# Optimization experiments

Measured on AMD Instinct MI355X. Metric: run time of the kernel, lower is better.

Reference implementation:

```python
import jax, jax.numpy as jnp
import numpy as np

B, L, QD, H, D = 2, 2048, 1024, 16, 64  # batch, seq, q_dim, heads, head_dim
INNER = H * D


def rms_norm(x, scale):
    # matches torch RMSNorm: mean over last dim in fp32, eps=1e-6, learned scale
    rrms = jax.lax.rsqrt(jnp.mean(x.astype(jnp.float32) ** 2, axis=-1, keepdims=True) + 1e-6)
    return (x * rrms).astype(x.dtype) * scale


def apply_rope(xq, xk, pe):
    # pe: [1,1,L,D//2,2,2] rotation-matrix pairs (FLUX-style)
    def rot(x):
        xs = x.reshape(*x.shape[:-1], D // 2, 1, 2)  # B H L D/2 1 2
        out = pe[..., 0] * xs[..., 0] + pe[..., 1] * xs[..., 1]  # B H L D/2 2
        return out.reshape(x.shape).astype(x.dtype)
    return rot(xq), rot(xk)


def setup_inputs() -> dict:
    key = jax.random.key(0)
    ks = jax.random.split(key, 6)
    s = 0.02
    return {
        "x": jax.random.normal(ks[0], (B, L, QD), jnp.float32),
        "pe": jax.random.normal(ks[1], (1, 1, L, D // 2, 2, 2), jnp.float32),
        "Wq": jax.random.normal(ks[2], (INNER, QD), jnp.float32) * s,
        "Wkv": jax.random.normal(ks[3], (2 * INNER, QD), jnp.float32) * s,
        "Wproj": jax.random.normal(ks[4], (QD, INNER), jnp.float32) * s,
        "bproj": jnp.zeros((QD,), jnp.float32),
        "q_scale": jnp.ones((D,), jnp.float32),
        "k_scale": jnp.ones((D,), jnp.float32),
    }


def reference(x, pe, Wq, Wkv, Wproj, bproj, q_scale, k_scale):
    # q/kv projections (self-attention: context = x)
    q = jnp.einsum('blc,ec->ble', x, Wq).reshape(B, L, H, D).transpose(0, 2, 1, 3)  # B H L D
    kv = jnp.einsum('blc,ec->ble', x, Wkv).reshape(B, L, 2, H, D)  # layout (K H D)
    k = kv[:, :, 0].transpose(0, 2, 1, 3)  # B H L D
    v = kv[:, :, 1].transpose(0, 2, 1, 3)  # B H L D
    # per-head QK RMSNorm
    q = rms_norm(q, q_scale)
    k = rms_norm(k, k_scale)
    # RoPE then scaled dot-product attention
    q, k = apply_rope(q, k, pe)
    scores = jnp.einsum('bhqd,bhkd->bhqk', q, k) / np.float32(np.sqrt(D))
    attn = jax.nn.softmax(scores, axis=-1)
    o = jnp.einsum('bhqk,bhkd->bhqd', attn, v)
    o = o.transpose(0, 2, 1, 3).reshape(B, L, INNER)  # B L (H D)
    return o @ Wproj.T + bproj
```

## Files before the change

### kernel.cpp

```cpp
#include <hip/hip_runtime.h>
#include <hip/hip_bf16.h>
#include <stdint.h>

#define BB 2
#define LL 2048
#define QDIM 1024
#define NH 16
#define HD 64

using bf16x8 = __attribute__((ext_vector_type(8))) __bf16;
using f32x4  = __attribute__((ext_vector_type(4))) float;
using u16x8  = __attribute__((ext_vector_type(8))) unsigned short;
using u32x2  = __attribute__((ext_vector_type(2))) uint32_t;

__device__ __forceinline__ unsigned short f2bf(float f) {
  uint32_t u = __builtin_bit_cast(uint32_t, f);
  u = (u + 0x7fffu + ((u >> 16) & 1u)) >> 16;
  return (unsigned short)u;
}
__device__ __forceinline__ float bf2f(unsigned short h) {
  uint32_t u = ((uint32_t)h) << 16;
  return __builtin_bit_cast(float, u);
}

__device__ __forceinline__ void gload_lds16(const void* g, void* l) {
  __builtin_amdgcn_global_load_lds((__attribute__((address_space(1))) void*)g,
                                   (__attribute__((address_space(3))) void*)l,
                                   16, 0, 0);
}

__global__ __launch_bounds__(256) void k_cast_bf16(const float* __restrict__ in,
                                                   unsigned short* __restrict__ out, int n) {
  int i = (blockIdx.x * 256 + threadIdx.x) * 8;
  if (i >= n) return;
  float4 a = *reinterpret_cast<const float4*>(in + i);
  float4 b = *reinterpret_cast<const float4*>(in + i + 4);
  u16x8 o;
  o[0] = f2bf(a.x); o[1] = f2bf(a.y); o[2] = f2bf(a.z); o[3] = f2bf(a.w);
  o[4] = f2bf(b.x); o[5] = f2bf(b.y); o[6] = f2bf(b.z); o[7] = f2bf(b.w);
  *reinterpret_cast<u16x8*>(out + i) = o;
}

template <int MODE>
__global__ __launch_bounds__(256) void k_gemm_bt(const unsigned short* __restrict__ A,
                                                 const unsigned short* __restrict__ Bw,
                                                 unsigned short* __restrict__ Cb,
                                                 float* __restrict__ Cf,
                                                 unsigned short* __restrict__ vT,
                                                 const float* __restrict__ bias,
                                                 int K, int ldc) {
  __shared__ unsigned short As[128 * 32];
  __shared__ unsigned short Bs[128 * 32];
  const int t = threadIdx.x;
  const int lane = t & 63, w = t >> 6;
  const int wm = w >> 1, wn = w & 1;
  const int g = lane >> 4, r16 = lane & 15;
  const size_t am0 = (size_t)blockIdx.x * 128;
  const size_t bn0 = (size_t)blockIdx.y * 128;

  f32x4 acc[4][4] = {};

  const int o0 = t * 16;
  const int row0 = o0 >> 6, cb0 = o0 & 63;
  const int o1 = 4096 + t * 16;
  const int row1 = o1 >> 6, cb1 = o1 & 63;

  for (int kb = 0; kb < K; kb += 32) {
    __syncthreads();
    gload_lds16(A  + (am0 + row0) * K + kb + (cb0 >> 1), (char*)As + o0);
    gload_lds16(A  + (am0 + row1) * K + kb + (cb1 >> 1), (char*)As + o1);
    gload_lds16(Bw + (bn0 + row0) * K + kb + (cb0 >> 1), (char*)Bs + o0);
    gload_lds16(Bw + (bn0 + row1) * K + kb + (cb1 >> 1), (char*)Bs + o1);
    __syncthreads();

    bf16x8 af[4], bfr[4];
#pragma unroll
    for (int i = 0; i < 4; ++i)
      af[i] = *reinterpret_cast<const bf16x8*>((const char*)As + (wm * 64 + i * 16 + r16) * 64 + g * 16);
#pragma unroll
    for (int j = 0; j < 4; ++j)
      bfr[j] = *reinterpret_cast<const bf16x8*>((const char*)Bs + (wn * 64 + j * 16 + r16) * 64 + g * 16);
#pragma unroll
    for (int i = 0; i < 4; ++i)
#pragma unroll
      for (int j = 0; j < 4; ++j)
        acc[i][j] = __builtin_amdgcn_mfma_f32_16x16x32_bf16(af[i], bfr[j], acc[i][j], 0, 0, 0);
  }

#pragma unroll
  for (int i = 0; i < 4; ++i)
#pragma unroll
    for (int j = 0; j < 4; ++j) {
      size_t row = am0 + wm * 64 + i * 16 + g * 4;
      int col = (int)bn0 + wn * 64 + j * 16 + r16;
      if (MODE == 2) {
#pragma unroll
        for (int r = 0; r < 4; ++r) Cf[(row + r) * ldc + col] = acc[i][j][r] + bias[col];
      } else if (MODE == 0) {
#pragma unroll
        for (int r = 0; r < 4; ++r) Cb[(row + r) * ldc + col] = f2bf(acc[i][j][r]);
      } else {
        if (col < 1024) {
#pragma unroll
          for (int r = 0; r < 4; ++r) Cb[(row + r) * 2048 + 1024 + col] = f2bf(acc[i][j][r]);
        } else {
          int e = col - 1024, h = e >> 6, d = e & 63;
          int b = (int)(row >> 11), l2 = (int)(row & 2047);
          ushort4 pk;
          pk.x = f2bf(acc[i][j][0]); pk.y = f2bf(acc[i][j][1]);
          pk.z = f2bf(acc[i][j][2]); pk.w = f2bf(acc[i][j][3]);
          *reinterpret_cast<ushort4*>(vT + ((size_t)(b * 16 + h) * 64 + d) * 2048 + l2) = pk;
        }
      }
    }
}

__global__ __launch_bounds__(256) void k_norm_rope(unsigned short* __restrict__ qkbuf,
                                                   const float* __restrict__ pe,
                                                   const float* __restrict__ qs,
                                                   const float* __restrict__ ks) {
  const int row = blockIdx.x;
  const int l = row & (LL - 1);
  const int t = threadIdx.x, w = t >> 6, lane = t & 63;
  const int hgrp = lane >> 5, dp = lane & 31;
  const size_t base = (size_t)row * 2048;
  const float4 pev = *reinterpret_cast<const float4*>(pe + ((size_t)l * 32 + dp) * 4);
  const float2 qsv = *reinterpret_cast<const float2*>(qs + dp * 2);
  const float2 ksv = *reinterpret_cast<const float2*>(ks + dp * 2);

#pragma unroll
  for (int pass = 0; pass < 4; ++pass) {
    const int isK = pass >> 1;
    const int h = w * 4 + (pass & 1) * 2 + hgrp;
    unsigned short* p = qkbuf + base + isK * 1024 + h * 64 + dp * 2;
    uint32_t v = *reinterpret_cast<uint32_t*>(p);
    float xe = bf2f((unsigned short)(v & 0xffff)), xo = bf2f((unsigned short)(v >> 16));
    float s = xe * xe + xo * xo;
#pragma unroll
    for (int mk = 1; mk < 32; mk <<= 1) s += __shfl_xor(s, mk);
    float rr = rsqrtf(s * (1.0f / 64.0f) + 1e-6f);
    float sx = isK ? ksv.x : qsv.x, sy = isK ? ksv.y : qsv.y;
    float ne = xe * rr * sx, no = xo * rr * sy;
    float oe = pev.x * ne + pev.y * no;
    float oo = pev.z * ne + pev.w * no;
    *reinterpret_cast<uint32_t*>(p) = (uint32_t)f2bf(oe) | ((uint32_t)f2bf(oo) << 16);
  }
}

__global__ __launch_bounds__(256, 4) void k_flash(const unsigned short* __restrict__ qkbuf,
                                                  const unsigned short* __restrict__ vT,
                                                  unsigned short* __restrict__ ob) {
  __shared__ unsigned short Plds[4][16][64];
  __shared__ unsigned short Ktile[2][64 * 64];
  __shared__ unsigned short Vtile[2][64 * 64];
  const int t = threadIdx.x, w = t >> 6, lane = t & 63;
  const int g = lane >> 4, r16 = lane & 15;
  const int id = blockIdx.x;
  const int bh = (id & 7) + (((id >> 3) & 3) << 3);
  const int lt = id >> 5;
  const int b = bh >> 4, h = bh & 15;
  const int l0 = lt * 64 + w * 16;
  const size_t qkb = (size_t)b * LL * 2048;
  const unsigned short* Qp = qkbuf + qkb + (size_t)(l0 + r16) * 2048 + h * 64;
  const unsigned short* Kbase = qkbuf + qkb + 1024 + h * 64;
  const unsigned short* Vbase = vT + (size_t)bh * 64 * 2048;

  const bf16x8 qf0 = *reinterpret_cast<const bf16x8*>(Qp + g * 8);
  const bf16x8 qf1 = *reinterpret_cast<const bf16x8*>(Qp + 32 + g * 8);

  f32x4 oacc[4] = {};
  float m = -1e30f, lsum = 0.f;

  char* Pw = (char*)&Plds[w][0][0];
  const int pswz = (r16 & 7) << 4;
  const int prow = r16 * 128;
  const int wr0 = prow + ((0 * 32 + g * 8) ^ pswz);
  const int wr1 = prow + ((1 * 32 + g * 8) ^ pswz);
  const int wr2 = prow + ((2 * 32 + g * 8) ^ pswz);
  const int wr3 = prow + ((3 * 32 + g * 8) ^ pswz);
  const int rd0 = prow + ((g * 16) ^ pswz);
  const int rd1 = prow + ((64 + g * 16) ^ pswz);

  const int so0 = t * 16, sr0 = so0 >> 7, sl0 = (so0 & 127) ^ ((sr0 & 7) << 4);
  const int so1 = 4096 + t * 16, sr1 = so1 >> 7, sl1 = (so1 & 127) ^ ((sr1 & 7) << 4);

  gload_lds16(Kbase + (size_t)sr0 * 2048 + (sl0 >> 1), (char*)&Ktile[0][0] + so0);
  gload_lds16(Kbase + (size_t)sr1 * 2048 + (sl1 >> 1), (char*)&Ktile[0][0] + so1);
  gload_lds16(Vbase + (size_t)sr0 * 2048 + (sl0 >> 1), (char*)&Vtile[0][0] + so0);
  gload_lds16(Vbase + (size_t)sr1 * 2048 + (sl1 >> 1), (char*)&Vtile[0][0] + so1);
  __syncthreads();

  const int kswz = (r16 & 7) << 4;

  for (int kt = 0; kt < LL; kt += 64) {
    const int cur = (kt >> 6) & 1;
    if (kt + 64 < LL) {
      const int nxt = cur ^ 1;
      gload_lds16(Kbase + (size_t)(kt + 64 + sr0) * 2048 + (sl0 >> 1), (char*)&Ktile[nxt][0] + so0);
      gload_lds16(Kbase + (size_t)(kt + 64 + sr1) * 2048 + (sl1 >> 1), (char*)&Ktile[nxt][0] + so1);
      gload_lds16(Vbase + (size_t)sr0 * 2048 + kt + 64 + (sl0 >> 1), (char*)&Vtile[nxt][0] + so0);
      gload_lds16(Vbase + (size_t)sr1 * 2048 + kt + 64 + (sl1 >> 1), (char*)&Vtile[nxt][0] + so1);
    }
    const char* Kt = (const char*)&Ktile[cur][0];
    const char* Vt = (const char*)&Vtile[cur][0];

    f32x4 s[4];
#pragma unroll
    for (int kb = 0; kb < 4; ++kb) {
      const char* kp = Kt + (kb * 16 + r16) * 128;
      bf16x8 ka0 = *reinterpret_cast<const bf16x8*>(kp + ((g * 16) ^ kswz));
      bf16x8 ka1 = *reinterpret_cast<const bf16x8*>(kp + ((64 + g * 16) ^ kswz));
      f32x4 z = {};
      z = __builtin_amdgcn_mfma_f32_16x16x32_bf16(ka0, qf0, z, 0, 0, 0);
      z = __builtin_amdgcn_mfma_f32_16x16x32_bf16(ka1, qf1, z, 0, 0, 0);
      s[kb] = z;
    }
    float p[16];
#pragma unroll
    for (int kb = 0; kb < 4; ++kb)
#pragma unroll
      for (int r = 0; r < 4; ++r) p[kb * 4 + r] = s[kb][r] * 0.125f;
    float tm = p[0];
#pragma unroll
    for (int i = 1; i < 16; ++i) tm = fmaxf(tm, p[i]);
    tm = fmaxf(tm, __shfl_xor(tm, 16));
    tm = fmaxf(tm, __shfl_xor(tm, 32));
    float nm = fmaxf(m, tm);
    float alpha = __expf(m - nm);
    m = nm;
    float ts = 0.f;
#pragma unroll
    for (int i = 0; i < 16; ++i) { p[i] = __expf(p[i] - nm); ts += p[i]; }
    ts += __shfl_xor(ts, 16);
    ts += __shfl_xor(ts, 32);
    lsum = lsum * alpha + ts;
#pragma unroll
    for (int dt = 0; dt < 4; ++dt) oacc[dt] *= alpha;
    {
      u32x2 wv;
      wv[0] = (uint32_t)f2bf(p[0])  | ((uint32_t)f2bf(p[1])  << 16);
      wv[1] = (uint32_t)f2bf(p[2])  | ((uint32_t)f2bf(p[3])  << 16);
      *reinterpret_cast<u32x2*>(Pw + wr0) = wv;
      wv[0] = (uint32_t)f2bf(p[4])  | ((uint32_t)f2bf(p[5])  << 16);
      wv[1] = (uint32_t)f2bf(p[6])  | ((uint32_t)f2bf(p[7])  << 16);
      *reinterpret_cast<u32x2*>(Pw + wr1) = wv;
      wv[0] = (uint32_t)f2bf(p[8])  | ((uint32_t)f2bf(p[9])  << 16);
      wv[1] = (uint32_t)f2bf(p[10]) | ((uint32_t)f2bf(p[11]) << 16);
      *reinterpret_cast<u32x2*>(Pw + wr2) = wv;
      wv[0] = (uint32_t)f2bf(p[12]) | ((uint32_t)f2bf(p[13]) << 16);
      wv[1] = (uint32_t)f2bf(p[14]) | ((uint32_t)f2bf(p[15]) << 16);
      *reinterpret_cast<u32x2*>(Pw + wr3) = wv;
    }
    __asm__ __volatile__("s_waitcnt lgkmcnt(0)" ::: "memory");
    bf16x8 pb0 = *reinterpret_cast<const bf16x8*>(Pw + rd0);
    bf16x8 pb1 = *reinterpret_cast<const bf16x8*>(Pw + rd1);
#pragma unroll
    for (int dt = 0; dt < 4; ++dt) {
      const char* vp = Vt + (dt * 16 + r16) * 128;
      bf16x8 va0 = *reinterpret_cast<const bf16x8*>(vp + ((g * 16) ^ kswz));
      bf16x8 va1 = *reinterpret_cast<const bf16x8*>(vp + ((64 + g * 16) ^ kswz));
      oacc[dt] = __builtin_amdgcn_mfma_f32_16x16x32_bf16(va0, pb0, oacc[dt], 0, 0, 0);
      oacc[dt] = __builtin_amdgcn_mfma_f32_16x16x32_bf16(va1, pb1, oacc[dt], 0, 0, 0);
    }
    __syncthreads();
  }

  const float inv = 1.0f / lsum;
  const size_t orow = (size_t)(b * LL + l0 + r16) * 1024 + h * 64;
#pragma unroll
  for (int dt = 0; dt < 4; ++dt) {
    ushort4 pk;
    pk.x = f2bf(oacc[dt][0] * inv); pk.y = f2bf(oacc[dt][1] * inv);
    pk.z = f2bf(oacc[dt][2] * inv); pk.w = f2bf(oacc[dt][3] * inv);
    *reinterpret_cast<ushort4*>(ob + orow + dt * 16 + g * 4) = pk;
  }
}

extern "C" void kernel_launch(void* const* d_in, const int* in_sizes, int n_in,
                              void* d_out, int out_size, void* d_ws, size_t ws_size,
                              hipStream_t stream) {
  const float* x     = (const float*)d_in[0];
  const float* pe    = (const float*)d_in[1];
  const float* Wq    = (const float*)d_in[2];
  const float* Wkv   = (const float*)d_in[3];
  const float* Wproj = (const float*)d_in[4];
  const float* bproj = (const float*)d_in[5];
  const float* qs    = (const float*)d_in[6];
  const float* ks    = (const float*)d_in[7];
  float* out = (float*)d_out;

  char* ws = (char*)d_ws;
  unsigned short* xb     = (unsigned short*)(ws);
  unsigned short* Wqb    = (unsigned short*)(ws + 8u  * 1024 * 1024);
  unsigned short* Wkvb   = (unsigned short*)(ws + 10u * 1024 * 1024);
  unsigned short* Wprojb = (unsigned short*)(ws + 14u * 1024 * 1024);
  unsigned short* qk     = (unsigned short*)(ws + 16u * 1024 * 1024);
  unsigned short* vT     = (unsigned short*)(ws + 32u * 1024 * 1024);
  unsigned short* ob     = (unsigned short*)(ws + 40u * 1024 * 1024);

  k_cast_bf16<<<4194304 / 2048, 256, 0, stream>>>(x, xb, 4194304);
  k_cast_bf16<<<1048576 / 2048, 256, 0, stream>>>(Wq, Wqb, 1048576);
  k_cast_bf16<<<2097152 / 2048, 256, 0, stream>>>(Wkv, Wkvb, 2097152);
  k_cast_bf16<<<1048576 / 2048, 256, 0, stream>>>(Wproj, Wprojb, 1048576);

  k_gemm_bt<0><<<dim3(32, 8),  256, 0, stream>>>(xb, Wqb,  qk, nullptr, nullptr, nullptr, 1024, 2048);
  k_gemm_bt<1><<<dim3(32, 16), 256, 0, stream>>>(xb, Wkvb, qk, nullptr, vT,      nullptr, 1024, 0);

  k_norm_rope<<<BB * LL, 256, 0, stream>>>(qk, pe, qs, ks);
  k_flash<<<1024, 256, 0, stream>>>(qk, vT, ob);

  k_gemm_bt<2><<<dim3(32, 8), 256, 0, stream>>>(ob, Wprojb, nullptr, out, nullptr, bproj, 1024, 1024);
}
```

Before: 253.4 us.

## Merge QKV GEMMs, retile projection GEMM, fold softmax scale and lazily rescale

The Q and KV projections now run as one GEMM over a concatenated weight buffer in a single launch, which removes a launch and improves grid fill. The output projection uses 64-row tiles so it launches more blocks. The 1/sqrt(D)*log2(e) factor is folded into the q RMSNorm scale, so the softmax uses exp2 with no per-score multiply. The running-max rescale of the accumulator is skipped unless the max grows by more than a threshold. bf16 conversion now uses hardware cast intrinsics, and the deferred max bounds exp values by 2^11, which risks precision or overflow in corner cases.

New measurement: 227.5 us. 10.2% less time.

```diff
diff --git a/kernel.cpp b/kernel.cpp
--- a/kernel.cpp
+++ b/kernel.cpp
@@ -9,18 +9,22 @@
 #define HD 64
 
 using bf16x8 = __attribute__((ext_vector_type(8))) __bf16;
+using bf16x2 = __attribute__((ext_vector_type(2))) __bf16;
+using bf16x4 = __attribute__((ext_vector_type(4))) __bf16;
 using f32x4  = __attribute__((ext_vector_type(4))) float;
 using u16x8  = __attribute__((ext_vector_type(8))) unsigned short;
 using u32x2  = __attribute__((ext_vector_type(2))) uint32_t;
 
 __device__ __forceinline__ unsigned short f2bf(float f) {
-  uint32_t u = __builtin_bit_cast(uint32_t, f);
-  u = (u + 0x7fffu + ((u >> 16) & 1u)) >> 16;
-  return (unsigned short)u;
+  return __builtin_bit_cast(unsigned short, (__bf16)f);
 }
 __device__ __forceinline__ float bf2f(unsigned short h) {
   uint32_t u = ((uint32_t)h) << 16;
   return __builtin_bit_cast(float, u);
+}
+__device__ __forceinline__ uint32_t pkbf2(float a, float b) {
+  bf16x2 v = { (__bf16)a, (__bf16)b };
+  return __builtin_bit_cast(uint32_t, v);
 }
 
 __device__ __forceinline__ void gload_lds16(const void* g, void* l) {
@@ -41,14 +45,10 @@
   *reinterpret_cast<u16x8*>(out + i) = o;
 }
 
-template <int MODE>
-__global__ __launch_bounds__(256) void k_gemm_bt(const unsigned short* __restrict__ A,
-                                                 const unsigned short* __restrict__ Bw,
-                                                 unsigned short* __restrict__ Cb,
-                                                 float* __restrict__ Cf,
-                                                 unsigned short* __restrict__ vT,
-                                                 const float* __restrict__ bias,
-                                                 int K, int ldc) {
+__global__ __launch_bounds__(256) void k_gemm_qkv(const unsigned short* __restrict__ A,
+                                                  const unsigned short* __restrict__ Bw,
+                                                  unsigned short* __restrict__ qk,
+                                                  unsigned short* __restrict__ vT) {
   __shared__ unsigned short As[128 * 32];
   __shared__ unsigned short Bs[128 * 32];
   const int t = threadIdx.x;
@@ -57,13 +57,12 @@
   const int g = lane >> 4, r16 = lane & 15;
   const size_t am0 = (size_t)blockIdx.x * 128;
   const size_t bn0 = (size_t)blockIdx.y * 128;
+  const int K = 1024;
 
   f32x4 acc[4][4] = {};
 
-  const int o0 = t * 16;
-  const int row0 = o0 >> 6, cb0 = o0 & 63;
-  const int o1 = 4096 + t * 16;
-  const int row1 = o1 >> 6, cb1 = o1 & 63;
+  const int o0 = t * 16, row0 = o0 >> 6, cb0 = o0 & 63;
+  const int o1 = 4096 + t * 16, row1 = o1 >> 6, cb1 = o1 & 63;
 
   for (int kb = 0; kb < K; kb += 32) {
     __syncthreads();
@@ -93,25 +92,69 @@
     for (int j = 0; j < 4; ++j) {
       size_t row = am0 + wm * 64 + i * 16 + g * 4;
       int col = (int)bn0 + wn * 64 + j * 16 + r16;
-      if (MODE == 2) {
-#pragma unroll
-        for (int r = 0; r < 4; ++r) Cf[(row + r) * ldc + col] = acc[i][j][r] + bias[col];
-      } else if (MODE == 0) {
-#pragma unroll
-        for (int r = 0; r < 4; ++r) Cb[(row + r) * ldc + col] = f2bf(acc[i][j][r]);
+      if (col < 2048) {
+#pragma unroll
+        for (int r = 0; r < 4; ++r) qk[(row + r) * 2048 + col] = f2bf(acc[i][j][r]);
       } else {
-        if (col < 1024) {
-#pragma unroll
-          for (int r = 0; r < 4; ++r) Cb[(row + r) * 2048 + 1024 + col] = f2bf(acc[i][j][r]);
-        } else {
-          int e = col - 1024, h = e >> 6, d = e & 63;
-          int b = (int)(row >> 11), l2 = (int)(row & 2047);
-          ushort4 pk;
-          pk.x = f2bf(acc[i][j][0]); pk.y = f2bf(acc[i][j][1]);
-          pk.z = f2bf(acc[i][j][2]); pk.w = f2bf(acc[i][j][3]);
-          *reinterpret_cast<ushort4*>(vT + ((size_t)(b * 16 + h) * 64 + d) * 2048 + l2) = pk;
-        }
+        int e = col - 2048, h = e >> 6, d = e & 63;
+        int b = (int)(row >> 11), l2 = (int)(row & 2047);
+        ushort4 pk;
+        pk.x = f2bf(acc[i][j][0]); pk.y = f2bf(acc[i][j][1]);
+        pk.z = f2bf(acc[i][j][2]); pk.w = f2bf(acc[i][j][3]);
+        *reinterpret_cast<ushort4*>(vT + ((size_t)(b * 16 + h) * 64 + d) * 2048 + l2) = pk;
       }
+    }
+}
+
+__global__ __launch_bounds__(256) void k_gemm_proj(const unsigned short* __restrict__ A,
+                                                   const unsigned short* __restrict__ Bw,
+                                                   float* __restrict__ Cf,
+                                                   const float* __restrict__ bias) {
+  __shared__ unsigned short As[64 * 32];
+  __shared__ unsigned short Bs[128 * 32];
+  const int t = threadIdx.x;
+  const int lane = t & 63, w = t >> 6;
+  const int wm = w >> 1, wn = w & 1;
+  const int g = lane >> 4, r16 = lane & 15;
+  const size_t am0 = (size_t)blockIdx.x * 64;
+  const size_t bn0 = (size_t)blockIdx.y * 128;
+  const int K = 1024;
+
+  f32x4 acc[2][4] = {};
+
+  const int oa = t * 16, rowa = oa >> 6, cba = oa & 63;
+  const int ob0 = t * 16, rowb0 = ob0 >> 6, cbb0 = ob0 & 63;
+  const int ob1 = 4096 + t * 16, rowb1 = ob1 >> 6, cbb1 = ob1 & 63;
+
+  for (int kb = 0; kb < K; kb += 32) {
+    __syncthreads();
+    gload_lds16(A  + (am0 + rowa)  * K + kb + (cba  >> 1), (char*)As + oa);
+    gload_lds16(Bw + (bn0 + rowb0) * K + kb + (cbb0 >> 1), (char*)Bs + ob0);
+    gload_lds16(Bw + (bn0 + rowb1) * K + kb + (cbb1 >> 1), (char*)Bs + ob1);
+    __syncthreads();
+
+    bf16x8 af[2], bfr[4];
+#pragma unroll
+    for (int i = 0; i < 2; ++i)
+      af[i] = *reinterpret_cast<const bf16x8*>((const char*)As + (wm * 32 + i * 16 + r16) * 64 + g * 16);
+#pragma unroll
+    for (int j = 0; j < 4; ++j)
+      bfr[j] = *reinterpret_cast<const bf16x8*>((const char*)Bs + (wn * 64 + j * 16 + r16) * 64 + g * 16);
+#pragma unroll
+    for (int i = 0; i < 2; ++i)
+#pragma unroll
+      for (int j = 0; j < 4; ++j)
+        acc[i][j] = __builtin_amdgcn_mfma_f32_16x16x32_bf16(af[i], bfr[j], acc[i][j], 0, 0, 0);
+  }
+
+#pragma unroll
+  for (int i = 0; i < 2; ++i)
+#pragma unroll
+    for (int j = 0; j < 4; ++j) {
+      size_t row = am0 + wm * 32 + i * 16 + g * 4;
+      int col = (int)bn0 + wn * 64 + j * 16 + r16;
+#pragma unroll
+      for (int r = 0; r < 4; ++r) Cf[(row + r) * 1024 + col] = acc[i][j][r] + bias[col];
     }
 }
 
@@ -119,14 +162,16 @@
                                                    const float* __restrict__ pe,
                                                    const float* __restrict__ qs,
                                                    const float* __restrict__ ks) {
+  const float S2 = 0.125f * 1.44269504f;
   const int row = blockIdx.x;
   const int l = row & (LL - 1);
   const int t = threadIdx.x, w = t >> 6, lane = t & 63;
   const int hgrp = lane >> 5, dp = lane & 31;
   const size_t base = (size_t)row * 2048;
   const float4 pev = *reinterpret_cast<const float4*>(pe + ((size_t)l * 32 + dp) * 4);
-  const float2 qsv = *reinterpret_cast<const float2*>(qs + dp * 2);
+  const float2 qsv0 = *reinterpret_cast<const float2*>(qs + dp * 2);
   const float2 ksv = *reinterpret_cast<const float2*>(ks + dp * 2);
+  const float2 qsv = { qsv0.x * S2, qsv0.y * S2 };
 
 #pragma unroll
   for (int pass = 0; pass < 4; ++pass) {
@@ -219,36 +264,35 @@
 #pragma unroll
     for (int kb = 0; kb < 4; ++kb)
 #pragma unroll
-      for (int r = 0; r < 4; ++r) p[kb * 4 + r] = s[kb][r] * 0.125f;
+      for (int r = 0; r < 4; ++r) p[kb * 4 + r] = s[kb][r];
     float tm = p[0];
 #pragma unroll
     for (int i = 1; i < 16; ++i) tm = fmaxf(tm, p[i]);
     tm = fmaxf(tm, __shfl_xor(tm, 16));
     tm = fmaxf(tm, __shfl_xor(tm, 32));
-    float nm = fmaxf(m, tm);
-    float alpha = __expf(m - nm);
-    m = nm;
+    if (!__all(tm <= m + 11.0f)) {
+      float nm = fmaxf(m, tm);
+      float alpha = __builtin_exp2f(m - nm);
+      lsum *= alpha;
+#pragma unroll
+      for (int dt = 0; dt < 4; ++dt) oacc[dt] *= alpha;
+      m = nm;
+    }
     float ts = 0.f;
 #pragma unroll
-    for (int i = 0; i < 16; ++i) { p[i] = __expf(p[i] - nm); ts += p[i]; }
+    for (int i = 0; i < 16; ++i) { p[i] = __builtin_exp2f(p[i] - m); ts += p[i]; }
     ts += __shfl_xor(ts, 16);
     ts += __shfl_xor(ts, 32);
-    lsum = lsum * alpha + ts;
-#pragma unroll
-    for (int dt = 0; dt < 4; ++dt) oacc[dt] *= alpha;
+    lsum += ts;
     {
       u32x2 wv;
-      wv[0] = (uint32_t)f2bf(p[0])  | ((uint32_t)f2bf(p[1])  << 16);
-      wv[1] = (uint32_t)f2bf(p[2])  | ((uint32_t)f2bf(p[3])  << 16);
+      wv[0] = pkbf2(p[0],  p[1]);  wv[1] = pkbf2(p[2],  p[3]);
       *reinterpret_cast<u32x2*>(Pw + wr0) = wv;
-      wv[0] = (uint32_t)f2bf(p[4])  | ((uint32_t)f2bf(p[5])  << 16);
-      wv[1] = (uint32_t)f2bf(p[6])  | ((uint32_t)f2bf(p[7])  << 16);
+      wv[0] = pkbf2(p[4],  p[5]);  wv[1] = pkbf2(p[6],  p[7]);
       *reinterpret_cast<u32x2*>(Pw + wr1) = wv;
-      wv[0] = (uint32_t)f2bf(p[8])  | ((uint32_t)f2bf(p[9])  << 16);
-      wv[1] = (uint32_t)f2bf(p[10]) | ((uint32_t)f2bf(p[11]) << 16);
+      wv[0] = pkbf2(p[8],  p[9]);  wv[1] = pkbf2(p[10], p[11]);
       *reinterpret_cast<u32x2*>(Pw + wr2) = wv;
-      wv[0] = (uint32_t)f2bf(p[12]) | ((uint32_t)f2bf(p[13]) << 16);
-      wv[1] = (uint32_t)f2bf(p[14]) | ((uint32_t)f2bf(p[15]) << 16);
+      wv[0] = pkbf2(p[12], p[13]); wv[1] = pkbf2(p[14], p[15]);
       *reinterpret_cast<u32x2*>(Pw + wr3) = wv;
     }
     __asm__ __volatile__("s_waitcnt lgkmcnt(0)" ::: "memory");
@@ -291,23 +335,21 @@
 
   char* ws = (char*)d_ws;
   unsigned short* xb     = (unsigned short*)(ws);
-  unsigned short* Wqb    = (unsigned short*)(ws + 8u  * 1024 * 1024);
-  unsigned short* Wkvb   = (unsigned short*)(ws + 10u * 1024 * 1024);
+  unsigned short* Wall   = (unsigned short*)(ws + 8u  * 1024 * 1024);
   unsigned short* Wprojb = (unsigned short*)(ws + 14u * 1024 * 1024);
   unsigned short* qk     = (unsigned short*)(ws + 16u * 1024 * 1024);
   unsigned short* vT     = (unsigned short*)(ws + 32u * 1024 * 1024);
   unsigned short* ob     = (unsigned short*)(ws + 40u * 1024 * 1024);
 
   k_cast_bf16<<<4194304 / 2048, 256, 0, stream>>>(x, xb, 4194304);
-  k_cast_bf16<<<1048576 / 2048, 256, 0, stream>>>(Wq, Wqb, 1048576);
-  k_cast_bf16<<<2097152 / 2048, 256, 0, stream>>>(Wkv, Wkvb, 2097152);
+  k_cast_bf16<<<1048576 / 2048, 256, 0, stream>>>(Wq, Wall, 1048576);
+  k_cast_bf16<<<2097152 / 2048, 256, 0, stream>>>(Wkv, Wall + 1048576, 2097152);
   k_cast_bf16<<<1048576 / 2048, 256, 0, stream>>>(Wproj, Wprojb, 1048576);
 
-  k_gemm_bt<0><<<dim3(32, 8),  256, 0, stream>>>(xb, Wqb,  qk, nullptr, nullptr, nullptr, 1024, 2048);
-  k_gemm_bt<1><<<dim3(32, 16), 256, 0, stream>>>(xb, Wkvb, qk, nullptr, vT,      nullptr, 1024, 0);
+  k_gemm_qkv<<<dim3(32, 24), 256, 0, stream>>>(xb, Wall, qk, vT);
 
   k_norm_rope<<<BB * LL, 256, 0, stream>>>(qk, pe, qs, ks);
   k_flash<<<1024, 256, 0, stream>>>(qk, vT, ob);
 
-  k_gemm_bt<2><<<dim3(32, 8), 256, 0, stream>>>(ob, Wprojb, nullptr, out, nullptr, bproj, 1024, 1024);
-}
+  k_gemm_proj<<<dim3(64, 8), 256, 0, stream>>>(ob, Wprojb, out, bproj);
+}
```
